# Kernel optimization log

Measured on AMD Instinct MI355X. Metric: run time of the kernel, lower is better.

## Reference

```python
import jax, jax.numpy as jnp
import numpy as np

THETA = 10000.0

def apply_rope(x, positions):
    # x: [B, H, S, D_head], positions: [S] int
    d = x.shape[-1]
    inv_freq = THETA ** (-jnp.arange(0, d, 2, dtype=jnp.float32) / d)  # [d/2]
    ang = positions.astype(jnp.float32)[:, None] * inv_freq[None, :]   # [S, d/2]
    cos, sin = jnp.cos(ang), jnp.sin(ang)                              # broadcast over B,H
    x1, x2 = x[..., 0::2], x[..., 1::2]
    r1 = x1 * cos - x2 * sin
    r2 = x1 * sin + x2 * cos
    return jnp.stack([r1, r2], axis=-1).reshape(x.shape)


def setup_inputs() -> dict:
    key = jax.random.key(0)
    ks = jax.random.split(key, 5)
    B, S, D = 4, 2048, 1024
    scale = 1.0 / np.sqrt(D)
    return {
        "x": jax.random.normal(ks[0], (B, S, D), dtype=jnp.float32),
        "Wq": jax.random.normal(ks[1], (D, D), dtype=jnp.float32) * scale,
        "Wk": jax.random.normal(ks[2], (D, D), dtype=jnp.float32) * scale,
        "Wv": jax.random.normal(ks[3], (D, D), dtype=jnp.float32) * scale,
        "Wo": jax.random.normal(ks[4], (D, D), dtype=jnp.float32) * scale,
        "token_positions": jnp.arange(S, dtype=jnp.int32),
    }


def reference(x, Wq, Wk, Wv, Wo, token_positions):
    B, S, D = x.shape
    H = 16
    hd = D // H
    # fused QKV projection (weights stored [out, in], y = x @ W^T, no bias)
    qkv_w = jnp.concatenate([Wq, Wk, Wv], axis=0)          # [3D, D]
    qkv = x @ qkv_w.T                                      # [B, S, 3D]
    q, k, v = jnp.split(qkv, 3, axis=-1)
    # [B, S, D] -> [B, H, S, hd]
    def split_heads(t):
        return t.reshape(B, S, H, hd).transpose(0, 2, 1, 3)
    q, k, v = split_heads(q), split_heads(k), split_heads(v)
    q = apply_rope(q, token_positions)
    k = apply_rope(k, token_positions)
    scores = jnp.einsum('bhqd,bhkd->bhqk', q, k) / jnp.sqrt(jnp.float32(hd))
    causal = jnp.tril(jnp.ones((S, S), dtype=bool))        # True = attend
    scores = jnp.where(causal[None, None], scores, -jnp.inf)
    attn = jax.nn.softmax(scores, axis=-1)
    out = jnp.einsum('bhqk,bhkd->bhqd', attn, v)           # [B, H, S, hd]
    out = out.transpose(0, 2, 1, 3).reshape(B, S, D)
    return out @ Wo.T
```

## Files before the change

### kernel.cpp

```cpp
#include <hip/hip_runtime.h>
#include <hip/hip_bf16.h>


typedef __bf16 bf16x8 __attribute__((ext_vector_type(8)));
typedef float f32x4 __attribute__((ext_vector_type(4)));
typedef unsigned short u16x8 __attribute__((ext_vector_type(8)));

#define DEV static __device__ __forceinline__

DEV unsigned short f2bf(float f) {
  unsigned int u = __builtin_bit_cast(unsigned int, f);
  u += 0x7FFFu + ((u >> 16) & 1u);
  return (unsigned short)(u >> 16);
}
DEV float bf2f(unsigned short h) {
  unsigned int u = ((unsigned int)h) << 16;
  return __builtin_bit_cast(float, u);
}
DEV bf16x8 ld_bf8(const unsigned short* p) {
  union { u16x8 u; bf16x8 b; } c;
  c.u = *reinterpret_cast<const u16x8*>(p);
  return c.b;
}
DEV unsigned int pk2(float a, float b) {
  unsigned int r;
  asm("v_cvt_pk_bf16_f32 %0, %1, %2" : "=v"(r) : "v"(a), "v"(b));
  return r;
}

DEV void gload_lds16(const unsigned short* src, unsigned short* dst) {
  __builtin_amdgcn_global_load_lds(
      (const __attribute__((address_space(1))) void*)src,
      (__attribute__((address_space(3))) void*)dst, 16, 0, 0);
}

DEV void stage_tile(const unsigned short* g, int ldg, unsigned short* lds,
                    int wave, int lane) {
  int rl = lane >> 3;
  int c16 = lane & 7;
#pragma unroll
  for (int i = 0; i < 4; ++i) {
    int row = i * 32 + wave * 8 + rl;
    int sc16 = c16 ^ (row & 7);
    const unsigned short* src = g + (size_t)row * ldg + sc16 * 8;
    unsigned short* dst = lds + (i * 32 + wave * 8) * 64;
    gload_lds16(src, dst);
  }
}

DEV bf16x8 lds_frag(const unsigned short* lds, int row, int c16) {
  return ld_bf8(lds + row * 64 + ((c16 ^ (row & 7)) << 3));
}

__global__ void k_f32_to_bf16(const float* __restrict__ in,
                              unsigned short* __restrict__ out, int n4) {
  int i = blockIdx.x * blockDim.x + threadIdx.x;
  if (i < n4) {
    float4 v = reinterpret_cast<const float4*>(in)[i];
    uint2 o;
    o.x = pk2(v.x, v.y);
    o.y = pk2(v.z, v.w);
    reinterpret_cast<uint2*>(out)[i] = o;
  }
}

__global__ void k_conv_w(const float* __restrict__ Wq, const float* __restrict__ Wk,
                         const float* __restrict__ Wv, const float* __restrict__ Wo,
                         unsigned short* __restrict__ Wb, unsigned short* __restrict__ Wob) {
  int i = blockIdx.x * blockDim.x + threadIdx.x;
  int which = i >> 18, j = i & 262143;
  const float* src = (which == 0) ? Wq : (which == 1) ? Wk : (which == 2) ? Wv : Wo;
  unsigned short* dst = (which == 3) ? Wob : Wb + (size_t)which * 1048576;
  float4 v = reinterpret_cast<const float4*>(src)[j];
  uint2 o;
  o.x = pk2(v.x, v.y);
  o.y = pk2(v.z, v.w);
  reinterpret_cast<uint2*>(dst)[j] = o;
}

__global__ void k_rope_table(const int* __restrict__ pos, float* __restrict__ tab) {
  int idx = blockIdx.x * blockDim.x + threadIdx.x;
  if (idx >= 2048 * 32) return;
  int s = idx >> 5, i = idx & 31;
  double inv = pow(10000.0, -(double)(2 * i) / 64.0);
  double ang = (double)pos[s] * inv;
  tab[idx * 2]     = (float)cos(ang);
  tab[idx * 2 + 1] = (float)sin(ang);
}

__global__ __launch_bounds__(256) void k_rope(unsigned short* __restrict__ Qh,
                                              unsigned short* __restrict__ Kh,
                                              const float* __restrict__ tab) {
  int idx = blockIdx.x * blockDim.x + threadIdx.x;
  int which = idx >> 20;
  int j = idx & 1048575;
  int db = (j & 7) * 8;
  int s = (j >> 3) & 2047;
  unsigned short* buf = which ? Kh : Qh;
  unsigned short* p = buf + (size_t)j * 8;
  uint4 v = *reinterpret_cast<const uint4*>(p);
  const float4* tp = reinterpret_cast<const float4*>(tab + s * 64 + db);
  float4 t0 = tp[0], t1 = tp[1];
  unsigned int r[4];
  float cs[4][2] = {{t0.x, t0.y}, {t0.z, t0.w}, {t1.x, t1.y}, {t1.z, t1.w}};
  unsigned int vv[4] = {v.x, v.y, v.z, v.w};
#pragma unroll
  for (int pq = 0; pq < 4; ++pq) {
    float x1 = bf2f((unsigned short)(vv[pq] & 0xFFFF));
    float x2 = bf2f((unsigned short)(vv[pq] >> 16));
    r[pq] = pk2(x1 * cs[pq][0] - x2 * cs[pq][1], x1 * cs[pq][1] + x2 * cs[pq][0]);
  }
  *reinterpret_cast<uint4*>(p) = make_uint4(r[0], r[1], r[2], r[3]);
}

__global__ __launch_bounds__(256) void k_gemm_qkv(
    const unsigned short* __restrict__ A, const unsigned short* __restrict__ W,
    unsigned short* __restrict__ Qh, unsigned short* __restrict__ Kh,
    unsigned short* __restrict__ Vt) {
  const int Kd = 1024, S = 2048;
  __shared__ __align__(16) unsigned short SM[128 * 132];
  unsigned short* As = SM;
  unsigned short* Bs = SM + 8192;
  int id = blockIdx.x;
  int xcd = id & 7, pos = id >> 3;
  int nid = xcd * 192 + pos;
  int nIdx = nid % 24, mIdx = nid / 24;
  int m0 = mIdx * 128, n0 = nIdx * 128;
  int wave = threadIdx.x >> 6, lane = threadIdx.x & 63;
  int wm = wave >> 1, wn = wave & 1;
  int lr = lane & 15, lk = lane >> 4;
  const unsigned short* Ag = A + (size_t)m0 * Kd;
  const unsigned short* Wg = W + (size_t)n0 * Kd;
  f32x4 acc[4][4] = {};
  for (int k0 = 0; k0 < Kd; k0 += 64) {
    stage_tile(Ag + k0, Kd, As, wave, lane);
    stage_tile(Wg + k0, Kd, Bs, wave, lane);
    __syncthreads();
#pragma unroll
    for (int ks = 0; ks < 2; ++ks) {
      bf16x8 a[4], b[4];
#pragma unroll
      for (int fm = 0; fm < 4; ++fm) a[fm] = lds_frag(As, wm * 64 + fm * 16 + lr, ks * 4 + lk);
#pragma unroll
      for (int fn = 0; fn < 4; ++fn) b[fn] = lds_frag(Bs, wn * 64 + fn * 16 + lr, ks * 4 + lk);
#pragma unroll
      for (int fm = 0; fm < 4; ++fm)
#pragma unroll
        for (int fn = 0; fn < 4; ++fn)
          acc[fm][fn] = __builtin_amdgcn_mfma_f32_16x16x32_bf16(a[fm], b[fn], acc[fm][fn], 0, 0, 0);
    }
    __syncthreads();
  }

  int t = nIdx >> 3;
  int b = m0 >> 11, s_base = m0 & 2047;
  if (t == 2) {
#pragma unroll
    for (int fm = 0; fm < 4; ++fm) {
      int r0 = wm * 64 + fm * 16 + lk * 4;
#pragma unroll
      for (int fn = 0; fn < 4; ++fn) {
        int c = wn * 64 + fn * 16 + lr;
        uint2 w;
        w.x = pk2(acc[fm][fn][0], acc[fm][fn][1]);
        w.y = pk2(acc[fm][fn][2], acc[fm][fn][3]);
        *reinterpret_cast<uint2*>(SM + c * 132 + r0) = w;
      }
    }
    __syncthreads();
    int h0 = (nIdx - 16) * 2;
#pragma unroll
    for (int it = 0; it < 16; ++it) {
      int idx2 = it * 256 + threadIdx.x;
      int c = idx2 >> 5, ch = idx2 & 31;
      int h = h0 + (c >> 6), d = c & 63;
      uint2 w = *reinterpret_cast<const uint2*>(SM + c * 132 + ch * 4);
      *reinterpret_cast<uint2*>(Vt + (((size_t)(b * 16 + h) * 64) + d) * S + s_base + ch * 4) = w;
    }
  } else {
    unsigned short* dst0 = (t == 0) ? Qh : Kh;
    int h0 = (nIdx & 7) * 2;
#pragma unroll
    for (int fm = 0; fm < 4; ++fm) {
      int r0 = wm * 64 + fm * 16 + lk * 4;
#pragma unroll
      for (int fn = 0; fn < 4; ++fn) {
        int c = wn * 64 + fn * 16 + lr;
        int h = h0 + (c >> 6), d = c & 63;
#pragma unroll
        for (int r = 0; r < 4; ++r) {
          int s = s_base + r0 + r;
          dst0[(((size_t)(b * 16 + h)) * S + s) * 64 + d] = f2bf(acc[fm][fn][r]);
        }
      }
    }
  }
}

__global__ __launch_bounds__(512) void k_attn(
    const unsigned short* __restrict__ Qh, const unsigned short* __restrict__ Kh,
    const unsigned short* __restrict__ Vt, unsigned short* __restrict__ Obuf) {
  const int S = 2048;
  const float KF = 0.18033688f;
  const float NEGH = -34.624667f;
  int bh = blockIdx.x;
  int b = bh >> 4, h = bh & 15;
  int wave = threadIdx.x >> 6, lane = threadIdx.x & 63;
  int lr = lane & 15, lk = lane >> 4;
  int yy = (int)gridDim.y - 1 - (int)blockIdx.y;
  int qt = 2 * yy + (wave >> 2);
  int q0 = qt * 128 + (wave & 3) * 32;
  const unsigned short* Qp = Qh + (size_t)bh * S * 64;
  const unsigned short* Kp = Kh + (size_t)bh * S * 64;
  const unsigned short* Vp = Vt + (size_t)bh * 64 * S;

  __shared__ __align__(16) unsigned short Ks[2][64 * 64];
  __shared__ __align__(16) unsigned short Vs[2][64 * 64];
  __shared__ __align__(16) unsigned short P_all[8][32][64];
  char* pw = (char*)&P_all[wave][0][0];

  auto STAGE = [&](int buf, int kv0) {
    int rl = lane >> 3, c16 = lane & 7;
    int row = wave * 8 + rl;
    int sc = (c16 ^ rl) << 3;
    gload_lds16(Kp + (size_t)(kv0 + row) * 64 + sc, &Ks[buf][wave * 8 * 64]);
    gload_lds16(Vp + (size_t)row * S + kv0 + sc,    &Vs[buf][wave * 8 * 64]);
  };

  bf16x8 qb[2][2];
#pragma unroll
  for (int mi = 0; mi < 2; ++mi)
#pragma unroll
    for (int ks = 0; ks < 2; ++ks)
      qb[mi][ks] = ld_bf8(Qp + (size_t)(q0 + mi * 16 + lr) * 64 + ks * 32 + lk * 8);

  f32x4 acc_o[4][2] = {};
  float l_run[2] = {0.f, 0.f};
  int my_nt = (q0 + 31) / 64 + 1;
  int NT = 2 * (2 * yy + 1) + 2;

  STAGE(0, 0);
  __syncthreads();

  for (int t = 0; t < NT; ++t) {
    int cur = t & 1;
    if (t + 1 < NT) STAGE(cur ^ 1, (t + 1) * 64);
    if (t < my_nt) {
      int kv0 = t * 64;
      bf16x8 ka[4][2];
#pragma unroll
      for (int ni = 0; ni < 4; ++ni)
#pragma unroll
        for (int ks = 0; ks < 2; ++ks)
          ka[ni][ks] = lds_frag(&Ks[cur][0], ni * 16 + lr, ks * 4 + lk);
      f32x4 st[4][2] = {};
      __builtin_amdgcn_s_setprio(1);
#pragma unroll
      for (int ni = 0; ni < 4; ++ni)
#pragma unroll
        for (int mi = 0; mi < 2; ++mi) {
          st[ni][mi] = __builtin_amdgcn_mfma_f32_16x16x32_bf16(ka[ni][0], qb[mi][0], st[ni][mi], 0, 0, 0);
          st[ni][mi] = __builtin_amdgcn_mfma_f32_16x16x32_bf16(ka[ni][1], qb[mi][1], st[ni][mi], 0, 0, 0);
        }
      __builtin_amdgcn_s_setprio(0);
      bf16x8 va[4][2];
#pragma unroll
      for (int nf = 0; nf < 4; ++nf)
#pragma unroll
        for (int ks = 0; ks < 2; ++ks)
          va[nf][ks] = lds_frag(&Vs[cur][0], nf * 16 + lr, ks * 4 + lk);

      if (kv0 + 63 > q0) {
#pragma unroll
        for (int mi = 0; mi < 2; ++mi) {
          int row = q0 + mi * 16 + lr;
#pragma unroll
          for (int ni = 0; ni < 4; ++ni)
#pragma unroll
            for (int r = 0; r < 4; ++r)
              if (kv0 + ni * 16 + lk * 4 + r > row) st[ni][mi][r] = -3e38f;
        }
      }
#pragma unroll
      for (int mi = 0; mi < 2; ++mi) {
        int prow = mi * 16 + lr;
        char* rowp = pw + prow * 128;
        int swz = (lr & 7) << 4;
        float rs = 0.f;
#pragma unroll
        for (int ni = 0; ni < 4; ++ni) {
          float p0 = __builtin_amdgcn_exp2f(fmaf(st[ni][mi][0], KF, NEGH));
          float p1 = __builtin_amdgcn_exp2f(fmaf(st[ni][mi][1], KF, NEGH));
          float p2 = __builtin_amdgcn_exp2f(fmaf(st[ni][mi][2], KF, NEGH));
          float p3 = __builtin_amdgcn_exp2f(fmaf(st[ni][mi][3], KF, NEGH));
          rs += (p0 + p1) + (p2 + p3);
          uint2 w; w.x = pk2(p0, p1); w.y = pk2(p2, p3);
          *reinterpret_cast<uint2*>(rowp + ((ni * 32 + lk * 8) ^ swz)) = w;
        }
        rs += __shfl_xor(rs, 16);
        rs += __shfl_xor(rs, 32);
        l_run[mi] += rs;
      }
      bf16x8 pb[2][2];
#pragma unroll
      for (int mi = 0; mi < 2; ++mi) {
        int prow = mi * 16 + lr;
        int swz = (lr & 7) << 4;
#pragma unroll
        for (int ks = 0; ks < 2; ++ks)
          pb[mi][ks] = ld_bf8((const unsigned short*)(pw + prow * 128 + ((ks * 64 + lk * 16) ^ swz)));
      }
      __builtin_amdgcn_s_setprio(1);
#pragma unroll
      for (int nf = 0; nf < 4; ++nf)
#pragma unroll
        for (int mi = 0; mi < 2; ++mi) {
          acc_o[nf][mi] = __builtin_amdgcn_mfma_f32_16x16x32_bf16(va[nf][0], pb[mi][0], acc_o[nf][mi], 0, 0, 0);
          acc_o[nf][mi] = __builtin_amdgcn_mfma_f32_16x16x32_bf16(va[nf][1], pb[mi][1], acc_o[nf][mi], 0, 0, 0);
        }
      __builtin_amdgcn_s_setprio(0);
    }
    __syncthreads();
  }

#pragma unroll
  for (int mi = 0; mi < 2; ++mi) {
    float inv_l = 1.f / l_run[mi];
    int q = q0 + mi * 16 + lr;
    size_t base = ((size_t)b * S + q) * 1024 + h * 64;
#pragma unroll
    for (int nf = 0; nf < 4; ++nf) {
      uint2 w;
      w.x = pk2(acc_o[nf][mi][0] * inv_l, acc_o[nf][mi][1] * inv_l);
      w.y = pk2(acc_o[nf][mi][2] * inv_l, acc_o[nf][mi][3] * inv_l);
      *reinterpret_cast<uint2*>(Obuf + base + nf * 16 + lk * 4) = w;
    }
  }
}

__global__ __launch_bounds__(256) void k_gemm_out(
    const unsigned short* __restrict__ A, const unsigned short* __restrict__ W,
    float* __restrict__ C) {
  const int Kd = 1024;
  __shared__ __align__(16) unsigned short As[128 * 64];
  __shared__ __align__(16) unsigned short Bs[128 * 64];
  int m0 = blockIdx.x * 128, n0 = blockIdx.y * 128;
  int wave = threadIdx.x >> 6, lane = threadIdx.x & 63;
  int wm = wave >> 1, wn = wave & 1;
  int lr = lane & 15, lk = lane >> 4;
  const unsigned short* Ag = A + (size_t)m0 * Kd;
  const unsigned short* Wg = W + (size_t)n0 * Kd;
  f32x4 acc[4][4] = {};
  for (int k0 = 0; k0 < Kd; k0 += 64) {
    stage_tile(Ag + k0, Kd, As, wave, lane);
    stage_tile(Wg + k0, Kd, Bs, wave, lane);
    __syncthreads();
#pragma unroll
    for (int ks = 0; ks < 2; ++ks) {
      bf16x8 a[4], b[4];
#pragma unroll
      for (int fm = 0; fm < 4; ++fm) a[fm] = lds_frag(As, wm * 64 + fm * 16 + lr, ks * 4 + lk);
#pragma unroll
      for (int fn = 0; fn < 4; ++fn) b[fn] = lds_frag(Bs, wn * 64 + fn * 16 + lr, ks * 4 + lk);
#pragma unroll
      for (int fm = 0; fm < 4; ++fm)
#pragma unroll
        for (int fn = 0; fn < 4; ++fn)
          acc[fm][fn] = __builtin_amdgcn_mfma_f32_16x16x32_bf16(a[fm], b[fn], acc[fm][fn], 0, 0, 0);
    }
    __syncthreads();
  }
#pragma unroll
  for (int fm = 0; fm < 4; ++fm)
#pragma unroll
    for (int fn = 0; fn < 4; ++fn)
#pragma unroll
      for (int r = 0; r < 4; ++r)
        C[(size_t)(m0 + wm * 64 + fm * 16 + lk * 4 + r) * 1024 + n0 + wn * 64 + fn * 16 + lr] =
            acc[fm][fn][r];
}

extern "C" void kernel_launch(void* const* d_in, const int* in_sizes, int n_in,
                              void* d_out, int out_size, void* d_ws, size_t ws_size,
                              hipStream_t stream) {
  const float* x  = (const float*)d_in[0];
  const float* Wq = (const float*)d_in[1];
  const float* Wk = (const float*)d_in[2];
  const float* Wv = (const float*)d_in[3];
  const float* Wo = (const float*)d_in[4];
  const int* pos  = (const int*)d_in[5];
  float* out = (float*)d_out;
  char* ws = (char*)d_ws;

  unsigned short* xb  = (unsigned short*)(ws);
  unsigned short* Wb  = (unsigned short*)(ws + 16777216);
  unsigned short* Wob = (unsigned short*)(ws + 23068672);
  unsigned short* Qh  = (unsigned short*)(ws + 25165824);
  unsigned short* Kh  = (unsigned short*)(ws + 41943040);
  unsigned short* Ob  = (unsigned short*)(ws + 58720256);
  unsigned short* Vt  = (unsigned short*)(ws + 75497472);
  float* tab          = (float*)(ws + 92274688);
  (void)in_sizes; (void)n_in; (void)out_size; (void)ws_size;

  k_f32_to_bf16<<<8192, 256, 0, stream>>>(x, xb, 2097152);
  k_conv_w<<<4096, 256, 0, stream>>>(Wq, Wk, Wv, Wo, Wb, Wob);
  k_rope_table<<<256, 256, 0, stream>>>(pos, tab);

  k_gemm_qkv<<<1536, 256, 0, stream>>>(xb, Wb, Qh, Kh, Vt);
  k_rope<<<8192, 256, 0, stream>>>(Qh, Kh, tab);
  dim3 ga(64, 8);
  k_attn<<<ga, 512, 0, stream>>>(Qh, Kh, Vt, Ob);
  dim3 g2(64, 8);
  k_gemm_out<<<g2, 256, 0, stream>>>(Ob, Wob, out);
}
```

Baseline: 183.5 us.

## Fuse RoPE into QKV GEMM epilogue and attention Q load; remap out-GEMM blocks

Removes the standalone RoPE kernel. K is rotated in the QKV GEMM epilogue using a lane shuffle to fetch the paired element, and Q is rotated as it is loaded into registers in the attention kernel. This saves a full read-modify-write pass over Q and K plus one kernel launch. The output GEMM also switches to a 1D grid with XCD-aware block remapping for better L2 locality. The risks are extra table loads in the epilogue and rounding to bf16 before rotating Q, which changes precision slightly.

New measurement: 169.9 us. 1.08x faster.

```diff
diff --git a/kernel.cpp b/kernel.cpp
--- a/kernel.cpp
+++ b/kernel.cpp
@@ -88,35 +88,10 @@
   tab[idx * 2 + 1] = (float)sin(ang);
 }
 
-__global__ __launch_bounds__(256) void k_rope(unsigned short* __restrict__ Qh,
-                                              unsigned short* __restrict__ Kh,
-                                              const float* __restrict__ tab) {
-  int idx = blockIdx.x * blockDim.x + threadIdx.x;
-  int which = idx >> 20;
-  int j = idx & 1048575;
-  int db = (j & 7) * 8;
-  int s = (j >> 3) & 2047;
-  unsigned short* buf = which ? Kh : Qh;
-  unsigned short* p = buf + (size_t)j * 8;
-  uint4 v = *reinterpret_cast<const uint4*>(p);
-  const float4* tp = reinterpret_cast<const float4*>(tab + s * 64 + db);
-  float4 t0 = tp[0], t1 = tp[1];
-  unsigned int r[4];
-  float cs[4][2] = {{t0.x, t0.y}, {t0.z, t0.w}, {t1.x, t1.y}, {t1.z, t1.w}};
-  unsigned int vv[4] = {v.x, v.y, v.z, v.w};
-#pragma unroll
-  for (int pq = 0; pq < 4; ++pq) {
-    float x1 = bf2f((unsigned short)(vv[pq] & 0xFFFF));
-    float x2 = bf2f((unsigned short)(vv[pq] >> 16));
-    r[pq] = pk2(x1 * cs[pq][0] - x2 * cs[pq][1], x1 * cs[pq][1] + x2 * cs[pq][0]);
-  }
-  *reinterpret_cast<uint4*>(p) = make_uint4(r[0], r[1], r[2], r[3]);
-}
-
 __global__ __launch_bounds__(256) void k_gemm_qkv(
     const unsigned short* __restrict__ A, const unsigned short* __restrict__ W,
     unsigned short* __restrict__ Qh, unsigned short* __restrict__ Kh,
-    unsigned short* __restrict__ Vt) {
+    unsigned short* __restrict__ Vt, const float* __restrict__ tab) {
   const int Kd = 1024, S = 2048;
   __shared__ __align__(16) unsigned short SM[128 * 132];
   unsigned short* As = SM;
@@ -177,8 +152,7 @@
       uint2 w = *reinterpret_cast<const uint2*>(SM + c * 132 + ch * 4);
       *reinterpret_cast<uint2*>(Vt + (((size_t)(b * 16 + h) * 64) + d) * S + s_base + ch * 4) = w;
     }
-  } else {
-    unsigned short* dst0 = (t == 0) ? Qh : Kh;
+  } else if (t == 1) {
     int h0 = (nIdx & 7) * 2;
 #pragma unroll
     for (int fm = 0; fm < 4; ++fm) {
@@ -187,10 +161,33 @@
       for (int fn = 0; fn < 4; ++fn) {
         int c = wn * 64 + fn * 16 + lr;
         int h = h0 + (c >> 6), d = c & 63;
+        int ri = d >> 1;
+        bool odd = d & 1;
 #pragma unroll
         for (int r = 0; r < 4; ++r) {
           int s = s_base + r0 + r;
-          dst0[(((size_t)(b * 16 + h)) * S + s) * 64 + d] = f2bf(acc[fm][fn][r]);
+          float2 cs = reinterpret_cast<const float2*>(tab)[s * 32 + ri];
+          float v = acc[fm][fn][r];
+          float other = __shfl_xor(v, 1);
+          float res = odd ? (other * cs.y + v * cs.x)
+                          : (v * cs.x - other * cs.y);
+          Kh[(((size_t)(b * 16 + h)) * S + s) * 64 + d] = f2bf(res);
+        }
+      }
+    }
+  } else {
+    int h0 = (nIdx & 7) * 2;
+#pragma unroll
+    for (int fm = 0; fm < 4; ++fm) {
+      int r0 = wm * 64 + fm * 16 + lk * 4;
+#pragma unroll
+      for (int fn = 0; fn < 4; ++fn) {
+        int c = wn * 64 + fn * 16 + lr;
+        int h = h0 + (c >> 6), d = c & 63;
+#pragma unroll
+        for (int r = 0; r < 4; ++r) {
+          int s = s_base + r0 + r;
+          Qh[(((size_t)(b * 16 + h)) * S + s) * 64 + d] = f2bf(acc[fm][fn][r]);
         }
       }
     }
@@ -199,7 +196,8 @@
 
 __global__ __launch_bounds__(512) void k_attn(
     const unsigned short* __restrict__ Qh, const unsigned short* __restrict__ Kh,
-    const unsigned short* __restrict__ Vt, unsigned short* __restrict__ Obuf) {
+    const unsigned short* __restrict__ Vt, unsigned short* __restrict__ Obuf,
+    const float* __restrict__ tab) {
   const int S = 2048;
   const float KF = 0.18033688f;
   const float NEGH = -34.624667f;
@@ -231,8 +229,23 @@
 #pragma unroll
   for (int mi = 0; mi < 2; ++mi)
 #pragma unroll
-    for (int ks = 0; ks < 2; ++ks)
-      qb[mi][ks] = ld_bf8(Qp + (size_t)(q0 + mi * 16 + lr) * 64 + ks * 32 + lk * 8);
+    for (int ks = 0; ks < 2; ++ks) {
+      int s = q0 + mi * 16 + lr;
+      int d0 = ks * 32 + lk * 8;
+      uint4 v = *reinterpret_cast<const uint4*>(Qp + (size_t)s * 64 + d0);
+      const float4* tp = reinterpret_cast<const float4*>(tab + s * 64 + d0);
+      float4 t0 = tp[0], t1 = tp[1];
+      float cs[4][2] = {{t0.x, t0.y}, {t0.z, t0.w}, {t1.x, t1.y}, {t1.z, t1.w}};
+      unsigned int vv[4] = {v.x, v.y, v.z, v.w};
+      union { unsigned int u[4]; bf16x8 bv; } r;
+#pragma unroll
+      for (int pq = 0; pq < 4; ++pq) {
+        float x1 = bf2f((unsigned short)(vv[pq] & 0xFFFF));
+        float x2 = bf2f((unsigned short)(vv[pq] >> 16));
+        r.u[pq] = pk2(x1 * cs[pq][0] - x2 * cs[pq][1], x1 * cs[pq][1] + x2 * cs[pq][0]);
+      }
+      qb[mi][ks] = r.bv;
+    }
 
   f32x4 acc_o[4][2] = {};
   float l_run[2] = {0.f, 0.f};
@@ -344,7 +357,11 @@
   const int Kd = 1024;
   __shared__ __align__(16) unsigned short As[128 * 64];
   __shared__ __align__(16) unsigned short Bs[128 * 64];
-  int m0 = blockIdx.x * 128, n0 = blockIdx.y * 128;
+  int id = blockIdx.x;
+  int xcd = id & 7, pos = id >> 3;
+  int nid = xcd * 64 + pos;
+  int nIdx = nid & 7, mIdx = nid >> 3;
+  int m0 = mIdx * 128, n0 = nIdx * 128;
   int wave = threadIdx.x >> 6, lane = threadIdx.x & 63;
   int wm = wave >> 1, wn = wave & 1;
   int lr = lane & 15, lk = lane >> 4;
@@ -406,10 +423,8 @@
   k_conv_w<<<4096, 256, 0, stream>>>(Wq, Wk, Wv, Wo, Wb, Wob);
   k_rope_table<<<256, 256, 0, stream>>>(pos, tab);
 
-  k_gemm_qkv<<<1536, 256, 0, stream>>>(xb, Wb, Qh, Kh, Vt);
-  k_rope<<<8192, 256, 0, stream>>>(Qh, Kh, tab);
+  k_gemm_qkv<<<1536, 256, 0, stream>>>(xb, Wb, Qh, Kh, Vt, tab);
   dim3 ga(64, 8);
-  k_attn<<<ga, 512, 0, stream>>>(Qh, Kh, Vt, Ob);
-  dim3 g2(64, 8);
-  k_gemm_out<<<g2, 256, 0, stream>>>(Ob, Wob, out);
-}
+  k_attn<<<ga, 512, 0, stream>>>(Qh, Kh, Vt, Ob, tab);
+  k_gemm_out<<<512, 256, 0, stream>>>(Ob, Wob, out);
+}
```
